# Kernel tuning notes

Measured on AMD Instinct MI355X. Metric: run time of the kernel, lower is better.

Reference implementation:

```python
import jax, jax.numpy as jnp
import numpy as np
from jax import lax

B = 32768
IMG = 28
K = 3
OUT_HW = IMG - K + 1  # 26
FLAT = OUT_HW * OUT_HW  # 676
HID = 300
NCLS = 10


def setup_inputs() -> dict:
    key = jax.random.key(0)
    ks = jax.random.split(key, 8)
    x = jax.random.normal(ks[0], (B, IMG * IMG), dtype=jnp.float32)
    conv_w = jax.random.normal(ks[1], (K, K), dtype=jnp.float32) * 0.1
    # Linear params stored as (in, out) so forward is h @ W + b
    W1 = jax.random.normal(ks[2], (FLAT, HID), dtype=jnp.float32) * 0.04
    b1 = jnp.zeros((HID,), dtype=jnp.float32)
    W2 = jax.random.normal(ks[3], (HID, HID), dtype=jnp.float32) * 0.06
    b2 = jnp.zeros((HID,), dtype=jnp.float32)
    W3 = jax.random.normal(ks[4], (HID, NCLS), dtype=jnp.float32) * 0.06
    b3 = jnp.zeros((NCLS,), dtype=jnp.float32)
    return {"x": x, "conv_w": conv_w, "W1": W1, "b1": b1,
            "W2": W2, "b2": b2, "W3": W3, "b3": b3}


def reference(x, conv_w, W1, b1, W2, b2, W3, b3):
    b = x.shape[0]
    img = x.reshape(b, 1, IMG, IMG)  # NCHW
    # Valid cross-correlation with 3x3 kernel -> [B,1,26,26]
    y = lax.conv_general_dilated(
        img, conv_w[None, None, :, :], window_strides=(1, 1), padding="VALID",
        dimension_numbers=("NCHW", "OIHW", "NCHW"))
    h = y.reshape(b, FLAT)
    h = jax.nn.relu(h @ W1 + b1)
    h = jax.nn.relu(h @ W2 + b2)
    return h @ W3 + b3
```

## Files before the change

kernel.cpp:

```cpp
#include <hip/hip_runtime.h>


typedef __bf16 bf16_t;
typedef __bf16 bf16x8 __attribute__((ext_vector_type(8)));
typedef float  f32x4  __attribute__((ext_vector_type(4)));

#define MFMA16(a, b, c) __builtin_amdgcn_mfma_f32_16x16x32_bf16((a), (b), (c), 0, 0, 0)

#define W1F_ELEMS (25 * 20 * 64 * 8)
#define W2F_ELEMS (10 * 20 * 64 * 8)
#define W3F_ELEMS (10 * 1 * 64 * 8)

#define SLOT_BYTES 16384

__global__ void prep_weights(const float* __restrict__ conv_w,
                             const float* __restrict__ W1,
                             const float* __restrict__ W2,
                             const float* __restrict__ W3,
                             bf16_t* __restrict__ W1f,
                             bf16_t* __restrict__ W2f,
                             bf16_t* __restrict__ W3f) {
    int idx = blockIdx.x * 256 + threadIdx.x;
    if (idx < 800 * 320) {
        int k = idx / 320;
        int n = idx - k * 320;
        float v = 0.0f;
        if (k < 784 && n < 300) {
            int py = k / 28;
            int px = k - py * 28;
#pragma unroll
            for (int ky = 0; ky < 3; ++ky) {
                int oy = py - ky;
                if (oy < 0 || oy > 25) continue;
#pragma unroll
                for (int kx = 0; kx < 3; ++kx) {
                    int ox = px - kx;
                    if (ox < 0 || ox > 25) continue;
                    v += conv_w[ky * 3 + kx] * W1[(oy * 26 + ox) * 300 + n];
                }
            }
        }
        int kc = k >> 5, quad = (k >> 3) & 3, j = k & 7;
        int nt = n >> 4, nin = n & 15;
        W1f[(((kc * 20 + nt) * 64 + quad * 16 + nin) << 3) + j] = (bf16_t)v;
    } else if (idx < 800 * 320 + 320 * 320) {
        int i2 = idx - 800 * 320;
        int k = i2 / 320;
        int n = i2 - k * 320;
        float v = (k < 300 && n < 300) ? W2[k * 300 + n] : 0.0f;
        int kc = k >> 5, quad = (k >> 3) & 3, j = k & 7;
        int nt = n >> 4, nin = n & 15;
        W2f[(((kc * 20 + nt) * 64 + quad * 16 + nin) << 3) + j] = (bf16_t)v;
    } else if (idx < 800 * 320 + 320 * 320 + 320 * 16) {
        int i3 = idx - (800 * 320 + 320 * 320);
        int k = i3 / 16;
        int n = i3 - k * 16;
        float v = (k < 300 && n < 10) ? W3[k * 10 + n] : 0.0f;
        int kc = k >> 5, quad = (k >> 3) & 3, j = k & 7;
        W3f[(((kc * 64) + quad * 16 + n) << 3) + j] = (bf16_t)v;
    }
}

__device__ __forceinline__ void stage16(const void* g, void* l) {
    __builtin_amdgcn_global_load_lds(
        (const __attribute__((address_space(1))) void*)g,
        (__attribute__((address_space(3))) void*)l, 16, 0, 0);
}

__global__ __launch_bounds__(512, 4) void fused_mlp(
    const float* __restrict__ x, const float* __restrict__ b1,
    const float* __restrict__ b2, const float* __restrict__ b3,
    const bf16x8* __restrict__ W1f, const bf16x8* __restrict__ W2f,
    const bf16x8* __restrict__ W3f, float* __restrict__ out) {
    __shared__ __align__(16) unsigned char smem[3 * SLOT_BYTES];
    bf16x8* hbuf = (bf16x8*)smem;
    bf16_t* hb   = (bf16_t*)smem;

    const int tid = threadIdx.x;
    const int w   = tid >> 6;
    const int l   = tid & 63;
    const int q   = l >> 4;
    const int l15 = l & 15;
    const int r0  = blockIdx.x * 64;

    const bool t3    = (w < 4);
    const int  nt0   = t3 ? (w * 3) : (12 + (w - 4) * 2);
    const int  boff2 = t3 ? 128 : 64;

    f32x4 acc[4][3];
#pragma unroll
    for (int m = 0; m < 4; ++m)
#pragma unroll
        for (int j = 0; j < 3; ++j) acc[m][j] = (f32x4){0.f, 0.f, 0.f, 0.f};

    const bf16x8* bB1 = W1f + nt0 * 64 + l;

#define STAGE_BAND(BAND)                                                       \
    {                                                                          \
        unsigned char* slot_ = smem + ((BAND) % 3) * SLOT_BYTES;               \
        if ((BAND) < 12) {                                                     \
            _Pragma("unroll")                                                  \
            for (int i_ = 0; i_ < 2; ++i_) {                                   \
                int row_ = w * 8 + i_ * 4 + (l >> 4);                          \
                int u_   = (l & 15) ^ (row_ & 7);                              \
                stage16(x + (size_t)(r0 + row_) * 784 + (BAND) * 64 + u_ * 4,  \
                        slot_ + w * 2048 + i_ * 1024);                         \
            }                                                                  \
        } else {                                                               \
            int row_ = w * 8 + (l >> 3);                                       \
            int u_   = (l & 7) ^ (row_ & 7);                                   \
            const float* src_ = x + (size_t)(r0 + row_) * 784 +                \
                                ((u_ < 4) ? (768 + u_ * 4) : 0);               \
            stage16(src_, slot_ + w * 1024);                                   \
        }                                                                      \
    }

#define AFRAG(DST, SLOT, RS, KCL, MT)                                          \
    {                                                                          \
        int row_ = (MT) * 16 + l15;                                            \
        int r7_  = row_ & 7;                                                   \
        float4 fa_ = *(const float4*)((SLOT) + row_ * (RS) +                   \
                     ((((KCL) * 8 + q * 2 + 0) ^ r7_) << 4));                  \
        float4 fb_ = *(const float4*)((SLOT) + row_ * (RS) +                   \
                     ((((KCL) * 8 + q * 2 + 1) ^ r7_) << 4));                  \
        bf16x8 t_;                                                             \
        t_[0] = (bf16_t)fa_.x; t_[1] = (bf16_t)fa_.y;                          \
        t_[2] = (bf16_t)fa_.z; t_[3] = (bf16_t)fa_.w;                          \
        t_[4] = (bf16_t)fb_.x; t_[5] = (bf16_t)fb_.y;                          \
        t_[6] = (bf16_t)fb_.z; t_[7] = (bf16_t)fb_.w;                          \
        DST = t_;                                                              \
    }

#define G1CHUNK(SLOT, RS, KCL, KC)                                             \
    {                                                                          \
        bf16x8 a0, a1, a2, a3;                                                 \
        AFRAG(a0, SLOT, RS, KCL, 0) AFRAG(a1, SLOT, RS, KCL, 1)                \
        AFRAG(a2, SLOT, RS, KCL, 2) AFRAG(a3, SLOT, RS, KCL, 3)                \
        const bf16x8* bp = bB1 + (KC) * 1280;                                  \
        bf16x8 b0 = bp[0], b1v = bp[64], b2v = bp[boff2];                      \
        acc[0][0] = MFMA16(a0, b0, acc[0][0]);                                 \
        acc[1][0] = MFMA16(a1, b0, acc[1][0]);                                 \
        acc[2][0] = MFMA16(a2, b0, acc[2][0]);                                 \
        acc[3][0] = MFMA16(a3, b0, acc[3][0]);                                 \
        acc[0][1] = MFMA16(a0, b1v, acc[0][1]);                                \
        acc[1][1] = MFMA16(a1, b1v, acc[1][1]);                                \
        acc[2][1] = MFMA16(a2, b1v, acc[2][1]);                                \
        acc[3][1] = MFMA16(a3, b1v, acc[3][1]);                                \
        if (t3) {                                                              \
            acc[0][2] = MFMA16(a0, b2v, acc[0][2]);                            \
            acc[1][2] = MFMA16(a1, b2v, acc[1][2]);                            \
            acc[2][2] = MFMA16(a2, b2v, acc[2][2]);                            \
            acc[3][2] = MFMA16(a3, b2v, acc[3][2]);                            \
        }                                                                      \
    }

#define VMW(N) asm volatile("s_waitcnt vmcnt(" #N ") lgkmcnt(0)" ::: "memory")
#define BARRIER()                         \
    __builtin_amdgcn_s_barrier();         \
    __builtin_amdgcn_sched_barrier(0)

    STAGE_BAND(0)
    STAGE_BAND(1)

    VMW(2);
    BARRIER();
    STAGE_BAND(2)
    __builtin_amdgcn_sched_barrier(0);
    {
        unsigned char* s0 = smem;
        G1CHUNK(s0, 256, 0, 0)
        G1CHUNK(s0, 256, 1, 1)
    }

    for (int band = 1; band <= 10; ++band) {
        if (t3) { VMW(8); } else { VMW(6); }
        BARRIER();
        STAGE_BAND(band + 2)
        __builtin_amdgcn_sched_barrier(0);
        unsigned char* sb = smem + (band % 3) * SLOT_BYTES;
        int kc = band * 2;
        G1CHUNK(sb, 256, 0, kc)
        G1CHUNK(sb, 256, 1, kc + 1)
    }

    if (t3) { VMW(7); } else { VMW(5); }
    BARRIER();
    {
        unsigned char* sb = smem + (11 % 3) * SLOT_BYTES;
        G1CHUNK(sb, 256, 0, 22)
        G1CHUNK(sb, 256, 1, 23)
    }

    if (t3) { VMW(6); } else { VMW(4); }
    BARRIER();
    {
        unsigned char* sb = smem + (12 % 3) * SLOT_BYTES;
        G1CHUNK(sb, 128, 0, 24)
    }

    asm volatile("s_waitcnt lgkmcnt(0)" ::: "memory");
    BARRIER();

#define HSTORE(J, BIAS)                                                        \
    {                                                                          \
        int n = (nt0 + (J)) * 16 + l15;                                        \
        float bias = (n < 300) ? (BIAS)[n] : 0.0f;                             \
        int kh = n >> 5, quad = (n >> 3) & 3, jj = n & 7;                      \
        _Pragma("unroll")                                                      \
        for (int mt = 0; mt < 4; ++mt)                                         \
            _Pragma("unroll")                                                  \
            for (int r = 0; r < 4; ++r) {                                      \
                float v = acc[mt][(J)][r] + bias;                              \
                v = v > 0.f ? v : 0.f;                                         \
                hb[(((kh * 4 + mt) * 64 + quad * 16 + q * 4 + r) << 3) + jj] = \
                    (bf16_t)v;                                                 \
            }                                                                  \
    }

    HSTORE(0, b1)
    HSTORE(1, b1)
    if (t3) HSTORE(2, b1)
    asm volatile("s_waitcnt lgkmcnt(0)" ::: "memory");
    BARRIER();

#pragma unroll
    for (int m = 0; m < 4; ++m)
#pragma unroll
        for (int j = 0; j < 3; ++j) acc[m][j] = (f32x4){0.f, 0.f, 0.f, 0.f};

    const bf16x8* bB2 = W2f + nt0 * 64 + l;

#define G2CHUNK(KC2)                                                           \
    {                                                                          \
        bf16x8 a0 = hbuf[((KC2) * 4 + 0) * 64 + l];                            \
        bf16x8 a1 = hbuf[((KC2) * 4 + 1) * 64 + l];                            \
        bf16x8 a2 = hbuf[((KC2) * 4 + 2) * 64 + l];                            \
        bf16x8 a3 = hbuf[((KC2) * 4 + 3) * 64 + l];                            \
        const bf16x8* bp = bB2 + (KC2) * 1280;                                 \
        bf16x8 b0 = bp[0], b1v = bp[64], b2v = bp[boff2];                      \
        acc[0][0] = MFMA16(a0, b0, acc[0][0]);                                 \
        acc[1][0] = MFMA16(a1, b0, acc[1][0]);                                 \
        acc[2][0] = MFMA16(a2, b0, acc[2][0]);                                 \
        acc[3][0] = MFMA16(a3, b0, acc[3][0]);                                 \
        acc[0][1] = MFMA16(a0, b1v, acc[0][1]);                                \
        acc[1][1] = MFMA16(a1, b1v, acc[1][1]);                                \
        acc[2][1] = MFMA16(a2, b1v, acc[2][1]);                                \
        acc[3][1] = MFMA16(a3, b1v, acc[3][1]);                                \
        if (t3) {                                                              \
            acc[0][2] = MFMA16(a0, b2v, acc[0][2]);                            \
            acc[1][2] = MFMA16(a1, b2v, acc[1][2]);                            \
            acc[2][2] = MFMA16(a2, b2v, acc[2][2]);                            \
            acc[3][2] = MFMA16(a3, b2v, acc[3][2]);                            \
        }                                                                      \
    }

    G2CHUNK(0) G2CHUNK(1) G2CHUNK(2) G2CHUNK(3) G2CHUNK(4)
    G2CHUNK(5) G2CHUNK(6) G2CHUNK(7) G2CHUNK(8) G2CHUNK(9)

    asm volatile("s_waitcnt lgkmcnt(0)" ::: "memory");
    BARRIER();

    HSTORE(0, b2)
    HSTORE(1, b2)
    if (t3) HSTORE(2, b2)
    asm volatile("s_waitcnt lgkmcnt(0)" ::: "memory");
    BARRIER();

    if (w < 4) {
        f32x4 acc3 = (f32x4){0.f, 0.f, 0.f, 0.f};
#pragma unroll
        for (int kc3 = 0; kc3 < 10; ++kc3)
            acc3 = MFMA16(hbuf[(kc3 * 4 + w) * 64 + l], W3f[kc3 * 64 + l], acc3);
        if (l15 < 10) {
            float bias = b3[l15];
#pragma unroll
            for (int r = 0; r < 4; ++r)
                out[(size_t)(r0 + w * 16 + q * 4 + r) * 10 + l15] = acc3[r] + bias;
        }
    }
}

extern "C" void kernel_launch(void* const* d_in, const int* in_sizes, int n_in,
                              void* d_out, int out_size, void* d_ws, size_t ws_size,
                              hipStream_t stream) {
    const float* x      = (const float*)d_in[0];
    const float* conv_w = (const float*)d_in[1];
    const float* W1     = (const float*)d_in[2];
    const float* b1     = (const float*)d_in[3];
    const float* W2     = (const float*)d_in[4];
    const float* b2     = (const float*)d_in[5];
    const float* W3     = (const float*)d_in[6];
    const float* b3     = (const float*)d_in[7];
    float* out = (float*)d_out;

    char* ws = (char*)d_ws;
    bf16_t* W1f = (bf16_t*)(ws);
    bf16_t* W2f = (bf16_t*)(ws + (size_t)W1F_ELEMS * 2);
    bf16_t* W3f = (bf16_t*)(ws + (size_t)(W1F_ELEMS + W2F_ELEMS) * 2);
    if (ws_size < (size_t)(W1F_ELEMS + W2F_ELEMS + W3F_ELEMS) * 2) return;

    int prep_total = 800 * 320 + 320 * 320 + 320 * 16;
    prep_weights<<<(prep_total + 255) / 256, 256, 0, stream>>>(
        conv_w, W1, W2, W3, W1f, W2f, W3f);

    fused_mlp<<<32768 / 64, 512, 0, stream>>>(
        x, b1, b2, b3, (const bf16x8*)W1f, (const bf16x8*)W2f,
        (const bf16x8*)W3f, out);
}
```

Before: 191.9 us.

## Stage W1 fragments through LDS with double-buffered pipeline alongside x bands

W1 B-fragments are now copied into a double-buffered LDS region with async global-to-LDS loads instead of each wave reading them straight from global memory. The x band pipeline shrinks from a triple to a double buffer so the two share LDS. The main loop interleaves W1 chunk staging with band staging and waits at a barrier per K-chunk. This aims to overlap weight fetch latency with MFMA work, at the cost of more barriers per iteration, shallower x prefetch depth and more LDS use (72KB), which may cut occupancy.

```diff
diff --git a/kernel.cpp b/kernel.cpp
--- a/kernel.cpp
+++ b/kernel.cpp
@@ -11,7 +11,8 @@
 #define W2F_ELEMS (10 * 20 * 64 * 8)
 #define W3F_ELEMS (10 * 1 * 64 * 8)
 
-#define SLOT_BYTES 16384
+#define XSLOT 16384
+#define XBASE 40960
 
 __global__ void prep_weights(const float* __restrict__ conv_w,
                              const float* __restrict__ W1,
@@ -72,7 +73,8 @@
     const float* __restrict__ b2, const float* __restrict__ b3,
     const bf16x8* __restrict__ W1f, const bf16x8* __restrict__ W2f,
     const bf16x8* __restrict__ W3f, float* __restrict__ out) {
-    __shared__ __align__(16) unsigned char smem[3 * SLOT_BYTES];
+    __shared__ __align__(16) unsigned char smem[XBASE + 2 * XSLOT];
+    bf16x8* Bb   = (bf16x8*)smem;
     bf16x8* hbuf = (bf16x8*)smem;
     bf16_t* hb   = (bf16_t*)smem;
 
@@ -93,17 +95,24 @@
 #pragma unroll
         for (int j = 0; j < 3; ++j) acc[m][j] = (f32x4){0.f, 0.f, 0.f, 0.f};
 
-    const bf16x8* bB1 = W1f + nt0 * 64 + l;
+#define STAGE_B(KC, BUF)                                                       \
+    {                                                                          \
+        const bf16x8* ws_ = W1f + (size_t)(KC)*1280 + l;                       \
+        bf16x8* wd_ = Bb + (BUF)*1280;                                         \
+        stage16(ws_ + w * 64, wd_ + w * 64);                                   \
+        stage16(ws_ + (w + 8) * 64, wd_ + (w + 8) * 64);                       \
+        if (w >= 4) stage16(ws_ + (w + 12) * 64, wd_ + (w + 12) * 64);         \
+    }
 
 #define STAGE_BAND(BAND)                                                       \
     {                                                                          \
-        unsigned char* slot_ = smem + ((BAND) % 3) * SLOT_BYTES;               \
+        unsigned char* slot_ = smem + XBASE + ((BAND)&1) * XSLOT;              \
         if ((BAND) < 12) {                                                     \
             _Pragma("unroll")                                                  \
             for (int i_ = 0; i_ < 2; ++i_) {                                   \
                 int row_ = w * 8 + i_ * 4 + (l >> 4);                          \
                 int u_   = (l & 15) ^ (row_ & 7);                              \
-                stage16(x + (size_t)(r0 + row_) * 784 + (BAND) * 64 + u_ * 4,  \
+                stage16(x + (size_t)(r0 + row_) * 784 + (BAND)*64 + u_ * 4,    \
                         slot_ + w * 2048 + i_ * 1024);                         \
             }                                                                  \
         } else {                                                               \
@@ -117,12 +126,12 @@
 
 #define AFRAG(DST, SLOT, RS, KCL, MT)                                          \
     {                                                                          \
-        int row_ = (MT) * 16 + l15;                                            \
+        int row_ = (MT)*16 + l15;                                              \
         int r7_  = row_ & 7;                                                   \
         float4 fa_ = *(const float4*)((SLOT) + row_ * (RS) +                   \
-                     ((((KCL) * 8 + q * 2 + 0) ^ r7_) << 4));                  \
+                     ((((KCL)*8 + q * 2 + 0) ^ r7_) << 4));                    \
         float4 fb_ = *(const float4*)((SLOT) + row_ * (RS) +                   \
-                     ((((KCL) * 8 + q * 2 + 1) ^ r7_) << 4));                  \
+                     ((((KCL)*8 + q * 2 + 1) ^ r7_) << 4));                    \
         bf16x8 t_;                                                             \
         t_[0] = (bf16_t)fa_.x; t_[1] = (bf16_t)fa_.y;                          \
         t_[2] = (bf16_t)fa_.z; t_[3] = (bf16_t)fa_.w;                          \
@@ -131,12 +140,107 @@
         DST = t_;                                                              \
     }
 
-#define G1CHUNK(SLOT, RS, KCL, KC)                                             \
+#define G1CHUNK(SLOT, RS, KCL, BUF)                                            \
     {                                                                          \
         bf16x8 a0, a1, a2, a3;                                                 \
         AFRAG(a0, SLOT, RS, KCL, 0) AFRAG(a1, SLOT, RS, KCL, 1)                \
         AFRAG(a2, SLOT, RS, KCL, 2) AFRAG(a3, SLOT, RS, KCL, 3)                \
-        const bf16x8* bp = bB1 + (KC) * 1280;                                  \
+        const bf16x8* bb_ = Bb + (BUF)*1280 + nt0 * 64 + l;                    \
+        bf16x8 b0 = bb_[0], b1v = bb_[64], b2v = bb_[boff2];                   \
+        acc[0][0] = MFMA16(a0, b0, acc[0][0]);                                 \
+        acc[1][0] = MFMA16(a1, b0, acc[1][0]);                                 \
+        acc[2][0] = MFMA16(a2, b0, acc[2][0]);                                 \
+        acc[3][0] = MFMA16(a3, b0, acc[3][0]);                                 \
+        acc[0][1] = MFMA16(a0, b1v, acc[0][1]);                                \
+        acc[1][1] = MFMA16(a1, b1v, acc[1][1]);                                \
+        acc[2][1] = MFMA16(a2, b1v, acc[2][1]);                                \
+        acc[3][1] = MFMA16(a3, b1v, acc[3][1]);                                \
+        if (t3) {                                                              \
+            acc[0][2] = MFMA16(a0, b2v, acc[0][2]);                            \
+            acc[1][2] = MFMA16(a1, b2v, acc[1][2]);                            \
+            acc[2][2] = MFMA16(a2, b2v, acc[2][2]);                            \
+            acc[3][2] = MFMA16(a3, b2v, acc[3][2]);                            \
+        }                                                                      \
+    }
+
+#define VMW(N) asm volatile("s_waitcnt vmcnt(" #N ") lgkmcnt(0)" ::: "memory")
+#define BARRIER()                         \
+    __builtin_amdgcn_s_barrier();         \
+    __builtin_amdgcn_sched_barrier(0)
+
+    STAGE_B(0, 0)
+    STAGE_BAND(0)
+    VMW(0);
+    BARRIER();
+
+    for (int b = 0; b <= 10; ++b) {
+        unsigned char* xs = smem + XBASE + (b & 1) * XSLOT;
+        const int k0 = 2 * b;
+        STAGE_B(k0 + 1, (k0 + 1) & 1)
+        STAGE_BAND(b + 1)
+        G1CHUNK(xs, 256, 0, k0 & 1)
+        VMW(2);
+        BARRIER();
+        STAGE_B(k0 + 2, (k0 + 2) & 1)
+        G1CHUNK(xs, 256, 1, (k0 + 1) & 1)
+        VMW(0);
+        BARRIER();
+    }
+    {
+        unsigned char* xs = smem + XBASE + XSLOT;
+        STAGE_B(23, 1)
+        STAGE_BAND(12)
+        G1CHUNK(xs, 256, 0, 0)
+        VMW(1);
+        BARRIER();
+        STAGE_B(24, 0)
+        G1CHUNK(xs, 256, 1, 1)
+        VMW(0);
+        BARRIER();
+    }
+    {
+        unsigned char* xs = smem + XBASE;
+        G1CHUNK(xs, 128, 0, 0)
+        asm volatile("s_waitcnt lgkmcnt(0)" ::: "memory");
+        BARRIER();
+    }
+
+#define HSTORE(J, BIAS)                                                        \
+    {                                                                          \
+        int n = (nt0 + (J)) * 16 + l15;                                        \
+        float bias = (n < 300) ? (BIAS)[n] : 0.0f;                             \
+        int kh = n >> 5, quad = (n >> 3) & 3, jj = n & 7;                      \
+        _Pragma("unroll")                                                      \
+        for (int mt = 0; mt < 4; ++mt)                                         \
+            _Pragma("unroll")                                                  \
+            for (int r = 0; r < 4; ++r) {                                      \
+                float v = acc[mt][(J)][r] + bias;                              \
+                v = v > 0.f ? v : 0.f;                                         \
+                hb[(((kh * 4 + mt) * 64 + quad * 16 + q * 4 + r) << 3) + jj] = \
+                    (bf16_t)v;                                                 \
+            }                                                                  \
+    }
+
+    HSTORE(0, b1)
+    HSTORE(1, b1)
+    if (t3) HSTORE(2, b1)
+    asm volatile("s_waitcnt lgkmcnt(0)" ::: "memory");
+    BARRIER();
+
+#pragma unroll
+    for (int m = 0; m < 4; ++m)
+#pragma unroll
+        for (int j = 0; j < 3; ++j) acc[m][j] = (f32x4){0.f, 0.f, 0.f, 0.f};
+
+    const bf16x8* bB2 = W2f + nt0 * 64 + l;
+
+#define G2CHUNK(KC2)                                                           \
+    {                                                                          \
+        bf16x8 a0 = hbuf[((KC2)*4 + 0) * 64 + l];                              \
+        bf16x8 a1 = hbuf[((KC2)*4 + 1) * 64 + l];                              \
+        bf16x8 a2 = hbuf[((KC2)*4 + 2) * 64 + l];                              \
+        bf16x8 a3 = hbuf[((KC2)*4 + 3) * 64 + l];                              \
+        const bf16x8* bp = bB2 + (KC2)*1280;                                   \
         bf16x8 b0 = bp[0], b1v = bp[64], b2v = bp[boff2];                      \
         acc[0][0] = MFMA16(a0, b0, acc[0][0]);                                 \
         acc[1][0] = MFMA16(a1, b0, acc[1][0]);                                 \
@@ -154,106 +258,6 @@
         }                                                                      \
     }
 
-#define VMW(N) asm volatile("s_waitcnt vmcnt(" #N ") lgkmcnt(0)" ::: "memory")
-#define BARRIER()                         \
-    __builtin_amdgcn_s_barrier();         \
-    __builtin_amdgcn_sched_barrier(0)
-
-    STAGE_BAND(0)
-    STAGE_BAND(1)
-
-    VMW(2);
-    BARRIER();
-    STAGE_BAND(2)
-    __builtin_amdgcn_sched_barrier(0);
-    {
-        unsigned char* s0 = smem;
-        G1CHUNK(s0, 256, 0, 0)
-        G1CHUNK(s0, 256, 1, 1)
-    }
-
-    for (int band = 1; band <= 10; ++band) {
-        if (t3) { VMW(8); } else { VMW(6); }
-        BARRIER();
-        STAGE_BAND(band + 2)
-        __builtin_amdgcn_sched_barrier(0);
-        unsigned char* sb = smem + (band % 3) * SLOT_BYTES;
-        int kc = band * 2;
-        G1CHUNK(sb, 256, 0, kc)
-        G1CHUNK(sb, 256, 1, kc + 1)
-    }
-
-    if (t3) { VMW(7); } else { VMW(5); }
-    BARRIER();
-    {
-        unsigned char* sb = smem + (11 % 3) * SLOT_BYTES;
-        G1CHUNK(sb, 256, 0, 22)
-        G1CHUNK(sb, 256, 1, 23)
-    }
-
-    if (t3) { VMW(6); } else { VMW(4); }
-    BARRIER();
-    {
-        unsigned char* sb = smem + (12 % 3) * SLOT_BYTES;
-        G1CHUNK(sb, 128, 0, 24)
-    }
-
-    asm volatile("s_waitcnt lgkmcnt(0)" ::: "memory");
-    BARRIER();
-
-#define HSTORE(J, BIAS)                                                        \
-    {                                                                          \
-        int n = (nt0 + (J)) * 16 + l15;                                        \
-        float bias = (n < 300) ? (BIAS)[n] : 0.0f;                             \
-        int kh = n >> 5, quad = (n >> 3) & 3, jj = n & 7;                      \
-        _Pragma("unroll")                                                      \
-        for (int mt = 0; mt < 4; ++mt)                                         \
-            _Pragma("unroll")                                                  \
-            for (int r = 0; r < 4; ++r) {                                      \
-                float v = acc[mt][(J)][r] + bias;                              \
-                v = v > 0.f ? v : 0.f;                                         \
-                hb[(((kh * 4 + mt) * 64 + quad * 16 + q * 4 + r) << 3) + jj] = \
-                    (bf16_t)v;                                                 \
-            }                                                                  \
-    }
-
-    HSTORE(0, b1)
-    HSTORE(1, b1)
-    if (t3) HSTORE(2, b1)
-    asm volatile("s_waitcnt lgkmcnt(0)" ::: "memory");
-    BARRIER();
-
-#pragma unroll
-    for (int m = 0; m < 4; ++m)
-#pragma unroll
-        for (int j = 0; j < 3; ++j) acc[m][j] = (f32x4){0.f, 0.f, 0.f, 0.f};
-
-    const bf16x8* bB2 = W2f + nt0 * 64 + l;
-
-#define G2CHUNK(KC2)                                                           \
-    {                                                                          \
-        bf16x8 a0 = hbuf[((KC2) * 4 + 0) * 64 + l];                            \
-        bf16x8 a1 = hbuf[((KC2) * 4 + 1) * 64 + l];                            \
-        bf16x8 a2 = hbuf[((KC2) * 4 + 2) * 64 + l];                            \
-        bf16x8 a3 = hbuf[((KC2) * 4 + 3) * 64 + l];                            \
-        const bf16x8* bp = bB2 + (KC2) * 1280;                                 \
-        bf16x8 b0 = bp[0], b1v = bp[64], b2v = bp[boff2];                      \
-        acc[0][0] = MFMA16(a0, b0, acc[0][0]);                                 \
-        acc[1][0] = MFMA16(a1, b0, acc[1][0]);                                 \
-        acc[2][0] = MFMA16(a2, b0, acc[2][0]);                                 \
-        acc[3][0] = MFMA16(a3, b0, acc[3][0]);                                 \
-        acc[0][1] = MFMA16(a0, b1v, acc[0][1]);                                \
-        acc[1][1] = MFMA16(a1, b1v, acc[1][1]);                                \
-        acc[2][1] = MFMA16(a2, b1v, acc[2][1]);                                \
-        acc[3][1] = MFMA16(a3, b1v, acc[3][1]);                                \
-        if (t3) {                                                              \
-            acc[0][2] = MFMA16(a0, b2v, acc[0][2]);                            \
-            acc[1][2] = MFMA16(a1, b2v, acc[1][2]);                            \
-            acc[2][2] = MFMA16(a2, b2v, acc[2][2]);                            \
-            acc[3][2] = MFMA16(a3, b2v, acc[3][2]);                            \
-        }                                                                      \
-    }
-
     G2CHUNK(0) G2CHUNK(1) G2CHUNK(2) G2CHUNK(3) G2CHUNK(4)
     G2CHUNK(5) G2CHUNK(6) G2CHUNK(7) G2CHUNK(8) G2CHUNK(9)
 
```

New measurement: 181.2 us. 1.06x faster.
